# Optimization experiments

Measured on AMD Instinct MI355X. Metric: run time of the kernel, lower is better.

The kernel has to match this reference:

```python
import jax, jax.numpy as jnp
import numpy as np

Q, L = 512, 4096


def setup_inputs() -> dict:
    key = jax.random.key(0)
    ks = jax.random.split(key, 12)
    def rn(k, shape, s=0.05):
        return jax.random.normal(k, shape, jnp.float32) * s
    return {
        "reactions": jax.random.normal(ks[0], (1, Q, 256), jnp.float32),
        "protein":   jax.random.normal(ks[1], (1, L, 1024), jnp.float32),
        # conv1d(1024->256, k=1) == pointwise linear
        "Wc":  rn(ks[2], (256, 1024)), "bc":  jnp.zeros((256,), jnp.float32),
        "W1":  rn(ks[3], (64, 256)),   "b1":  jnp.zeros((64,), jnp.float32),
        "W2":  rn(ks[4], (64, 256)),   "b2":  jnp.zeros((64,), jnp.float32),
        "Wa":  rn(ks[5], (64, 64)),    "ba":  jnp.zeros((64,), jnp.float32),
        "Wpa": rn(ks[6], (64, 64)),    "bpa": jnp.zeros((64,), jnp.float32),
        "Wra": rn(ks[7], (64, 64)),    "bra": jnp.zeros((64,), jnp.float32),
        "Wf1": rn(ks[8], (256, 128)),  "bf1": jnp.zeros((256,), jnp.float32),
        "Wf2": rn(ks[9], (128, 256)),  "bf2": jnp.zeros((128,), jnp.float32),
        "Wf3": rn(ks[10], (1, 128)),   "bf3": jnp.zeros((1,), jnp.float32),
    }


def reference(reactions, protein, Wc, bc, W1, b1, W2, b2, Wa, ba,
              Wpa, bpa, Wra, bra, Wf1, bf1, Wf2, bf2, Wf3, bf3):
    # protein: [1, L, 1024] -> 1x1 conv over channels == linear -> [L, 256]
    p = jax.nn.relu(protein[0] @ Wc.T + bc)
    # reactions: [1, Q, 256] -> [Q, 64]
    r = jax.nn.relu(reactions[0] @ W2.T + b2)
    # protein tokens -> [L, 64]
    k = jax.nn.relu(p @ W1.T + b1)

    ra = r @ Wra.T + bra            # [Q, 64]
    pa = k @ Wpa.T + bpa            # [L, 64]
    # broadcast outer-sum + relu + small linear: [Q, L, 64]
    A = jax.nn.relu(ra[:, None, :] + pa[None, :, :]) @ Wa.T + ba

    r_gate = jax.nn.sigmoid(jnp.mean(A, axis=1))   # [Q, 64]
    p_gate = jax.nn.sigmoid(jnp.mean(A, axis=0))   # [L, 64]

    rxnfp = r + r * r_gate                          # [Q, 64]
    prot = jnp.max(k + k * p_gate, axis=0)          # [64]  maxpool over L

    ctx = jnp.concatenate(
        [rxnfp, jnp.broadcast_to(prot, (rxnfp.shape[0], 64))], axis=1)  # [Q,128]

    # dropout layers are identity in eval mode
    h = jax.nn.leaky_relu(ctx @ Wf1.T + bf1)
    h = jax.nn.leaky_relu(h @ Wf2.T + bf2)
    out = h @ Wf3.T + bf3
    return out.reshape(-1)                          # [Q]
```

## Files before the change

### kernel.cpp

```cpp
#include <hip/hip_runtime.h>
#include <hip/hip_bf16.h>
#include <math.h>

#define TPB 256

typedef __attribute__((ext_vector_type(8))) short s16x8;
typedef __attribute__((ext_vector_type(4))) float f32x4;

#define MFMA16(a, b, c) __builtin_amdgcn_mfma_f32_16x16x32_bf16((a), (b), (c), 0, 0, 0)

constexpr unsigned OFF_P    = 0u;
constexpr unsigned OFF_K    = OFF_P    + 4096u*256u;
constexpr unsigned OFF_PA   = OFF_K    + 4096u*64u;
constexpr unsigned OFF_R    = OFF_PA   + 4096u*64u;
constexpr unsigned OFF_RA   = OFF_R    + 512u*64u;
constexpr unsigned OFF_SR   = OFF_RA   + 512u*64u;
constexpr unsigned OFF_PMAX = OFF_SR   + 512u*64u;

__device__ __forceinline__ short f2bf(float x) {
  union { float f; unsigned u; } v; v.f = x;
  unsigned r = v.u + 0x7FFFu + ((v.u >> 16) & 1u);
  return (short)(r >> 16);
}
__device__ __forceinline__ unsigned pkbf(float a, float b) {
  __hip_bfloat162 h = __float22bfloat162_rn(make_float2(a, b));
  union { __hip_bfloat162 h2; unsigned u; } v; v.h2 = h;
  return v.u;
}
union U8 { s16x8 s; unsigned u[4]; };

__global__ __launch_bounds__(TPB, 2) void k1_gemm(
    const float* __restrict__ prot, const float* __restrict__ Wc,
    const float* __restrict__ bc,   float* __restrict__ ws)
{
  int bid = blockIdx.x;
  int tid = threadIdx.x;
  if (bid >= 512) {
    int tb = bid - 512;
    unsigned base = OFF_SR + (unsigned)tb * 16384u;
#pragma unroll
    for (int it = 0; it < 16; ++it) {
      int idx = it * TPB + tid;
      *(float4*)&ws[base + (unsigned)idx * 4u] = make_float4(0.f, 0.f, 0.f, 0.f);
    }
    if (tb == 1 && tid < 16)
      *(float4*)&ws[OFF_PMAX + tid * 4] = make_float4(0.f, 0.f, 0.f, 0.f);
    return;
  }

  __shared__ __align__(16) short Asm[32 * 72];
  __shared__ __align__(16) short Bsm[64 * 72];

  int m0 = (bid >> 2) * 32;
  int n0 = (bid & 3) * 64;
  int wave = tid >> 6, lane = tid & 63;
  int wm = (wave & 1) * 16, wn = (wave >> 1) * 32;
  int lm = lane & 15, quad = lane >> 4;

  int arow = tid >> 3, aseg = (tid & 7) * 8;
  int brow = tid >> 2, bseg = (tid & 3) * 16;

  const float* Ag = prot + (size_t)(m0 + arow) * 1024 + aseg;
  const float* Bg = Wc   + (size_t)(n0 + brow) * 1024 + bseg;

  float4 a4[2], b4[4];
#pragma unroll
  for (int i = 0; i < 2; ++i) a4[i] = *(const float4*)(Ag + i * 4);
#pragma unroll
  for (int i = 0; i < 4; ++i) b4[i] = *(const float4*)(Bg + i * 4);

  f32x4 acc[2] = {};

  for (int kc = 0; kc < 16; ++kc) {
    __syncthreads();
    {
      U8 s;
      s.u[0] = pkbf(a4[0].x, a4[0].y); s.u[1] = pkbf(a4[0].z, a4[0].w);
      s.u[2] = pkbf(a4[1].x, a4[1].y); s.u[3] = pkbf(a4[1].z, a4[1].w);
      *(s16x8*)&Asm[arow * 72 + aseg] = s.s;
    }
#pragma unroll
    for (int h = 0; h < 2; ++h) {
      U8 s;
      s.u[0] = pkbf(b4[h*2].x,   b4[h*2].y);
      s.u[1] = pkbf(b4[h*2].z,   b4[h*2].w);
      s.u[2] = pkbf(b4[h*2+1].x, b4[h*2+1].y);
      s.u[3] = pkbf(b4[h*2+1].z, b4[h*2+1].w);
      *(s16x8*)&Bsm[brow * 72 + bseg + h * 8] = s.s;
    }
    if (kc < 15) {
#pragma unroll
      for (int i = 0; i < 2; ++i) a4[i] = *(const float4*)(Ag + (kc + 1) * 64 + i * 4);
#pragma unroll
      for (int i = 0; i < 4; ++i) b4[i] = *(const float4*)(Bg + (kc + 1) * 64 + i * 4);
    }
    __syncthreads();
#pragma unroll
    for (int ks = 0; ks < 2; ++ks) {
      s16x8 af = *(const s16x8*)&Asm[(wm + lm) * 72 + ks * 32 + quad * 8];
#pragma unroll
      for (int ni = 0; ni < 2; ++ni) {
        s16x8 bfv = *(const s16x8*)&Bsm[(wn + ni * 16 + lm) * 72 + ks * 32 + quad * 8];
        acc[ni] = MFMA16(af, bfv, acc[ni]);
      }
    }
  }

#pragma unroll
  for (int ni = 0; ni < 2; ++ni) {
    int col = n0 + wn + ni * 16 + lm;
    float bcv = bc[col];
#pragma unroll
    for (int r = 0; r < 4; ++r) {
      int row = m0 + wm + quad * 4 + r;
      ws[OFF_P + (unsigned)row * 256u + col] = fmaxf(acc[ni][r] + bcv, 0.f);
    }
  }
}

__global__ __launch_bounds__(TPB, 2) void k2_heads(
    const float* __restrict__ reactions,
    const float* __restrict__ W1,  const float* __restrict__ b1,
    const float* __restrict__ W2,  const float* __restrict__ b2,
    const float* __restrict__ Wpa, const float* __restrict__ bpa,
    const float* __restrict__ Wra, const float* __restrict__ bra,
    float* __restrict__ ws)
{
  __shared__ __align__(16) short Asm[32 * 264];
  __shared__ __align__(16) short Bsm[64 * 264];
  __shared__ __align__(16) short Ksm[32 * 72];
  __shared__ __align__(16) short Wsm[64 * 72];
  int bid = blockIdx.x, tid = threadIdx.x;
  bool isProt = bid < 128;
  int row0 = (isProt ? bid : (bid - 128)) * 32;
  const float* src  = isProt ? (ws + OFF_P) : reactions;
  const float* Wst1 = isProt ? W1 : W2;
  const float* bv   = isProt ? b1 : b2;
  const float* Wst2 = isProt ? Wpa : Wra;
  const float* b2nd = isProt ? bpa : bra;
  float* out1 = ws + (isProt ? OFF_K : OFF_R);
  float* out2 = ws + (isProt ? OFF_PA : OFF_RA);

  {
    int row = tid >> 3, seg = (tid & 7) * 32;
    const float* sp = src + (size_t)(row0 + row) * 256 + seg;
    float4 f[8];
#pragma unroll
    for (int i = 0; i < 8; ++i) f[i] = *(const float4*)(sp + i * 4);
#pragma unroll
    for (int i = 0; i < 4; ++i) {
      U8 s;
      s.u[0] = pkbf(f[2*i].x,   f[2*i].y);
      s.u[1] = pkbf(f[2*i].z,   f[2*i].w);
      s.u[2] = pkbf(f[2*i+1].x, f[2*i+1].y);
      s.u[3] = pkbf(f[2*i+1].z, f[2*i+1].w);
      *(s16x8*)&Asm[row * 264 + seg + i * 8] = s.s;
    }
  }
  {
    int row = tid >> 2, seg = (tid & 3) * 64;
    const float* sp = Wst1 + (size_t)row * 256 + seg;
#pragma unroll
    for (int i = 0; i < 8; ++i) {
      float4 fa = *(const float4*)(sp + i * 8);
      float4 fb = *(const float4*)(sp + i * 8 + 4);
      U8 s;
      s.u[0] = pkbf(fa.x, fa.y); s.u[1] = pkbf(fa.z, fa.w);
      s.u[2] = pkbf(fb.x, fb.y); s.u[3] = pkbf(fb.z, fb.w);
      *(s16x8*)&Bsm[row * 264 + seg + i * 8] = s.s;
    }
  }
  {
    int row = tid >> 2, seg = (tid & 3) * 16;
    const float* sp = Wst2 + (size_t)row * 64 + seg;
#pragma unroll
    for (int i = 0; i < 2; ++i) {
      float4 fa = *(const float4*)(sp + i * 8);
      float4 fb = *(const float4*)(sp + i * 8 + 4);
      U8 s;
      s.u[0] = pkbf(fa.x, fa.y); s.u[1] = pkbf(fa.z, fa.w);
      s.u[2] = pkbf(fb.x, fb.y); s.u[3] = pkbf(fb.z, fb.w);
      *(s16x8*)&Wsm[row * 72 + seg + i * 8] = s.s;
    }
  }
  __syncthreads();

  int wave = tid >> 6, lane = tid & 63;
  int lm = lane & 15, quad = lane >> 4;
  int wm = (wave >> 1) * 16, wn = (wave & 1) * 32;

  f32x4 acc[2] = {};
#pragma unroll
  for (int kc = 0; kc < 8; ++kc) {
    s16x8 a = *(const s16x8*)&Asm[(wm + lm) * 264 + kc * 32 + quad * 8];
#pragma unroll
    for (int ni = 0; ni < 2; ++ni) {
      s16x8 b = *(const s16x8*)&Bsm[(wn + ni * 16 + lm) * 264 + kc * 32 + quad * 8];
      acc[ni] = MFMA16(a, b, acc[ni]);
    }
  }
#pragma unroll
  for (int ni = 0; ni < 2; ++ni) {
    int col = wn + ni * 16 + lm;
    float bb = bv[col];
#pragma unroll
    for (int r = 0; r < 4; ++r) {
      int row = wm + quad * 4 + r;
      float kv = fmaxf(acc[ni][r] + bb, 0.f);
      out1[(size_t)(row0 + row) * 64 + col] = kv;
      Ksm[row * 72 + col] = f2bf(kv);
    }
  }
  __syncthreads();

  f32x4 acc2[2] = {};
#pragma unroll
  for (int kc = 0; kc < 2; ++kc) {
    s16x8 a = *(const s16x8*)&Ksm[(wm + lm) * 72 + kc * 32 + quad * 8];
#pragma unroll
    for (int ni = 0; ni < 2; ++ni) {
      s16x8 b = *(const s16x8*)&Wsm[(wn + ni * 16 + lm) * 72 + kc * 32 + quad * 8];
      acc2[ni] = MFMA16(a, b, acc2[ni]);
    }
  }
#pragma unroll
  for (int ni = 0; ni < 2; ++ni) {
    int col = wn + ni * 16 + lm;
    float bb = b2nd[col];
#pragma unroll
    for (int r = 0; r < 4; ++r) {
      int row = wm + quad * 4 + r;
      out2[(size_t)(row0 + row) * 64 + col] = acc2[ni][r] + bb;
    }
  }
}

__global__ __launch_bounds__(TPB, 4) void k3_interact(
    const float* __restrict__ Wa, const float* __restrict__ ba,
    float* __restrict__ ws)
{
  __shared__ float sm[8192];
  int bid = blockIdx.x, tid = threadIdx.x;
  int c = tid & 63, g = tid >> 6;
  const float* ra = ws + OFF_RA;
  const float* pa = ws + OFF_PA;

  if (bid < 256) {
    int l0 = bid * 16;
    float v[4], acc[4];
#pragma unroll
    for (int i = 0; i < 4; ++i) {
      v[i] = pa[(unsigned)(l0 + g * 4 + i) * 64u + c];
      acc[i] = 0.f;
    }
    const float* rap = ra + c;
#pragma unroll 8
    for (int q = 0; q < 512; ++q) {
      float x = rap[q * 64];
#pragma unroll
      for (int i = 0; i < 4; ++i) acc[i] += fmaxf(v[i] + x, 0.f);
    }
#pragma unroll
    for (int i = 0; i < 4; ++i) sm[(g * 4 + i) * 64 + c] = acc[i];
    for (int it = 0; it < 16; ++it) {
      int idx = it * TPB + tid;
      int a = idx >> 6, bb = idx & 63;
      sm[1024 + bb * 65 + a] = Wa[idx];
    }
    __syncthreads();
    float vmax = 0.f;
    float bac = ba[c];
#pragma unroll
    for (int i = 0; i < 4; ++i) {
      int ll = g * 4 + i;
      float dot = 0.f;
#pragma unroll 8
      for (int jj = 0; jj < 64; ++jj)
        dot += sm[ll * 64 + jj] * sm[1024 + jj * 65 + c];
      float pg = 1.f / (1.f + __expf(-(dot * (1.f / 512.f) + bac)));
      float val = ws[OFF_K + (unsigned)(l0 + ll) * 64u + c] * (1.f + pg);
      vmax = fmaxf(vmax, val);
    }
    atomicMax((int*)&ws[OFF_PMAX + c], __float_as_int(vmax));
  } else {
    int b = bid - 256;
    int qt = b >> 5, ls = b & 31;
    int q0 = qt * 16, l0 = ls * 128;
    int srow = tid >> 4, sc4 = (tid & 15) * 4;
    const float* src = pa + (size_t)l0 * 64;
#pragma unroll
    for (int it = 0; it < 8; ++it) {
      int row = it * 16 + srow;
      *(float4*)&sm[row * 64 + sc4] = *(const float4*)(src + row * 64 + sc4);
    }
    float u[4], acc[4];
#pragma unroll
    for (int i = 0; i < 4; ++i) {
      u[i] = ra[(unsigned)(q0 + g * 4 + i) * 64u + c];
      acc[i] = 0.f;
    }
    __syncthreads();
#pragma unroll 8
    for (int l = 0; l < 128; ++l) {
      float x = sm[l * 64 + c];
#pragma unroll
      for (int i = 0; i < 4; ++i) acc[i] += fmaxf(u[i] + x, 0.f);
    }
#pragma unroll
    for (int i = 0; i < 4; ++i)
      atomicAdd(&ws[OFF_SR + (unsigned)(q0 + g * 4 + i) * 64u + c], acc[i]);
  }
}

__global__ __launch_bounds__(TPB) void k4_final(
    const float* __restrict__ Wa,  const float* __restrict__ ba,
    const float* __restrict__ Wf1, const float* __restrict__ bf1,
    const float* __restrict__ Wf2, const float* __restrict__ bf2,
    const float* __restrict__ Wf3, const float* __restrict__ bf3,
    float* __restrict__ ws, float* __restrict__ out)
{
  __shared__ __align__(16) short mrb[16 * 72];
  __shared__ __align__(16) short wab[64 * 72];
  __shared__ __align__(16) short ctxb[16 * 136];
  __shared__ __align__(16) short h1b[16 * 264];
  __shared__ __align__(16) short wgt[256 * 136];
  __shared__ float red[64];
  int bid = blockIdx.x, tid = threadIdx.x;
  int q0 = bid * 16;
  int wave = tid >> 6, lane = tid & 63;
  int lm = lane & 15, quad = lane >> 4;

  {
    int q = tid >> 4, c4 = (tid & 15) * 4;
    float4 v = *(const float4*)&ws[OFF_SR + (unsigned)(q0 + q) * 64u + c4];
    uint2 st = make_uint2(pkbf(v.x * (1.f/4096.f), v.y * (1.f/4096.f)),
                          pkbf(v.z * (1.f/4096.f), v.w * (1.f/4096.f)));
    *(uint2*)&mrb[q * 72 + c4] = st;
  }
#pragma unroll
  for (int it = 0; it < 4; ++it) {
    int i4 = it * TPB + tid;
    int row = i4 >> 4, c4 = (i4 & 15) * 4;
    float4 v = *(const float4*)&Wa[row * 64 + c4];
    uint2 st = make_uint2(pkbf(v.x, v.y), pkbf(v.z, v.w));
    *(uint2*)&wab[row * 72 + c4] = st;
  }
  __syncthreads();

  f32x4 gacc = {};
#pragma unroll
  for (int kc = 0; kc < 2; ++kc) {
    s16x8 a = *(const s16x8*)&mrb[lm * 72 + kc * 32 + quad * 8];
    s16x8 b = *(const s16x8*)&wab[(wave * 16 + lm) * 72 + kc * 32 + quad * 8];
    gacc = MFMA16(a, b, gacc);
  }
  {
    int c = wave * 16 + lm;
    float bac = ba[c];
    short pb = f2bf(ws[OFF_PMAX + c]);
#pragma unroll
    for (int r = 0; r < 4; ++r) {
      int q = quad * 4 + r;
      float gg = 1.f / (1.f + __expf(-(gacc[r] + bac)));
      float rv = ws[OFF_R + (unsigned)(q0 + q) * 64u + c];
      ctxb[q * 136 + c]      = f2bf(rv * (1.f + gg));
      ctxb[q * 136 + 64 + c] = pb;
    }
  }
#pragma unroll 4
  for (int it = 0; it < 32; ++it) {
    int i4 = it * TPB + tid;
    int row = i4 >> 5, c4 = (i4 & 31) * 4;
    float4 v = *(const float4*)&Wf1[row * 128 + c4];
    uint2 st = make_uint2(pkbf(v.x, v.y), pkbf(v.z, v.w));
    *(uint2*)&wgt[row * 136 + c4] = st;
  }
  __syncthreads();

  f32x4 h[4] = {};
#pragma unroll
  for (int kc = 0; kc < 4; ++kc) {
    s16x8 a = *(const s16x8*)&ctxb[lm * 136 + kc * 32 + quad * 8];
#pragma unroll
    for (int nt = 0; nt < 4; ++nt) {
      s16x8 b = *(const s16x8*)&wgt[(wave * 64 + nt * 16 + lm) * 136 + kc * 32 + quad * 8];
      h[nt] = MFMA16(a, b, h[nt]);
    }
  }
#pragma unroll
  for (int nt = 0; nt < 4; ++nt) {
    int n = wave * 64 + nt * 16 + lm;
    float bb = bf1[n];
#pragma unroll
    for (int r = 0; r < 4; ++r) {
      int q = quad * 4 + r;
      float v = h[nt][r] + bb;
      v = v > 0.f ? v : 0.01f * v;
      h1b[q * 264 + n] = f2bf(v);
    }
  }
  __syncthreads();

#pragma unroll 4
  for (int it = 0; it < 32; ++it) {
    int i4 = it * TPB + tid;
    int row = i4 >> 6, c4 = (i4 & 63) * 4;
    float4 v = *(const float4*)&Wf2[row * 256 + c4];
    uint2 st = make_uint2(pkbf(v.x, v.y), pkbf(v.z, v.w));
    *(uint2*)&wgt[row * 264 + c4] = st;
  }
  __syncthreads();

  f32x4 o[2] = {};
#pragma unroll
  for (int kc = 0; kc < 8; ++kc) {
    s16x8 a = *(const s16x8*)&h1b[lm * 264 + kc * 32 + quad * 8];
#pragma unroll
    for (int nt = 0; nt < 2; ++nt) {
      s16x8 b = *(const s16x8*)&wgt[(wave * 32 + nt * 16 + lm) * 264 + kc * 32 + quad * 8];
      o[nt] = MFMA16(a, b, o[nt]);
    }
  }
  float pv[4] = {0.f, 0.f, 0.f, 0.f};
#pragma unroll
  for (int nt = 0; nt < 2; ++nt) {
    int m = wave * 32 + nt * 16 + lm;
    float bb = bf2[m], w3 = Wf3[m];
#pragma unroll
    for (int r = 0; r < 4; ++r) {
      float v = o[nt][r] + bb;
      v = v > 0.f ? v : 0.01f * v;
      pv[r] += v * w3;
    }
  }
#pragma unroll
  for (int msk = 1; msk < 16; msk <<= 1)
#pragma unroll
    for (int r = 0; r < 4; ++r) pv[r] += __shfl_xor(pv[r], msk);
  if (lm == 0) {
#pragma unroll
    for (int r = 0; r < 4; ++r) red[(quad * 4 + r) * 4 + wave] = pv[r];
  }
  __syncthreads();
  if (tid < 16)
    out[q0 + tid] = red[tid * 4] + red[tid * 4 + 1] + red[tid * 4 + 2] +
                    red[tid * 4 + 3] + bf3[0];
}

extern "C" void kernel_launch(void* const* d_in, const int* in_sizes, int n_in,
                              void* d_out, int out_size, void* d_ws, size_t ws_size,
                              hipStream_t stream)
{
  const float* reactions = (const float*)d_in[0];
  const float* protein   = (const float*)d_in[1];
  const float* Wc  = (const float*)d_in[2];
  const float* bc  = (const float*)d_in[3];
  const float* W1  = (const float*)d_in[4];
  const float* b1  = (const float*)d_in[5];
  const float* W2  = (const float*)d_in[6];
  const float* b2  = (const float*)d_in[7];
  const float* Wa  = (const float*)d_in[8];
  const float* ba  = (const float*)d_in[9];
  const float* Wpa = (const float*)d_in[10];
  const float* bpa = (const float*)d_in[11];
  const float* Wra = (const float*)d_in[12];
  const float* bra = (const float*)d_in[13];
  const float* Wf1 = (const float*)d_in[14];
  const float* bf1 = (const float*)d_in[15];
  const float* Wf2 = (const float*)d_in[16];
  const float* bf2 = (const float*)d_in[17];
  const float* Wf3 = (const float*)d_in[18];
  const float* bf3 = (const float*)d_in[19];
  float* ws  = (float*)d_ws;
  float* out = (float*)d_out;

  hipLaunchKernelGGL(k1_gemm, dim3(514), dim3(TPB), 0, stream,
                     protein, Wc, bc, ws);
  hipLaunchKernelGGL(k2_heads, dim3(144), dim3(TPB), 0, stream,
                     reactions, W1, b1, W2, b2, Wpa, bpa, Wra, bra, ws);
  hipLaunchKernelGGL(k3_interact, dim3(1280), dim3(TPB), 0, stream,
                     Wa, ba, ws);
  hipLaunchKernelGGL(k4_final, dim3(32), dim3(TPB), 0, stream,
                     Wa, ba, Wf1, bf1, Wf2, bf2, Wf3, bf3, ws, out);
}
```

Before: 172.9 us.

## Split p-gate reduction into balanced tiled atomic blocks plus separate gate kernel

Previously 256 blocks each looped over all 512 queries serially to compute per-L sums, giving long-tail, unbalanced blocks next to the tiled Q-sum blocks. The interaction kernel now uses one uniform tiled block type for both the Q-side and L-side sums, accumulated with atomics into a new zeroed workspace region. The gate/maxpool step moves into a new small kernel. This improves load balance and parallelism, at the cost of an extra kernel launch, more atomics and extra zeroing work in k1.

```diff
diff --git a/kernel.cpp b/kernel.cpp
--- a/kernel.cpp
+++ b/kernel.cpp
@@ -16,6 +16,7 @@
 constexpr unsigned OFF_RA   = OFF_R    + 512u*64u;
 constexpr unsigned OFF_SR   = OFF_RA   + 512u*64u;
 constexpr unsigned OFF_PMAX = OFF_SR   + 512u*64u;
+constexpr unsigned OFF_SP   = OFF_PMAX + 64u;
 
 __device__ __forceinline__ short f2bf(float x) {
   union { float f; unsigned u; } v; v.f = x;
@@ -37,14 +38,23 @@
   int tid = threadIdx.x;
   if (bid >= 512) {
     int tb = bid - 512;
-    unsigned base = OFF_SR + (unsigned)tb * 16384u;
-#pragma unroll
-    for (int it = 0; it < 16; ++it) {
-      int idx = it * TPB + tid;
-      *(float4*)&ws[base + (unsigned)idx * 4u] = make_float4(0.f, 0.f, 0.f, 0.f);
-    }
-    if (tb == 1 && tid < 16)
-      *(float4*)&ws[OFF_PMAX + tid * 4] = make_float4(0.f, 0.f, 0.f, 0.f);
+    if (tb < 2) {
+      unsigned base = OFF_SR + (unsigned)tb * 16384u;
+#pragma unroll
+      for (int it = 0; it < 16; ++it) {
+        int idx = it * TPB + tid;
+        *(float4*)&ws[base + (unsigned)idx * 4u] = make_float4(0.f, 0.f, 0.f, 0.f);
+      }
+      if (tb == 1 && tid < 16)
+        *(float4*)&ws[OFF_PMAX + tid * 4] = make_float4(0.f, 0.f, 0.f, 0.f);
+    } else {
+      unsigned base = OFF_SP + (unsigned)(tb - 2) * 32768u;
+#pragma unroll
+      for (int it = 0; it < 32; ++it) {
+        int idx = it * TPB + tid;
+        *(float4*)&ws[base + (unsigned)idx * 4u] = make_float4(0.f, 0.f, 0.f, 0.f);
+      }
+    }
     return;
   }
 
@@ -235,9 +245,7 @@
   }
 }
 
-__global__ __launch_bounds__(TPB, 4) void k3_interact(
-    const float* __restrict__ Wa, const float* __restrict__ ba,
-    float* __restrict__ ws)
+__global__ __launch_bounds__(TPB, 4) void k3_interact(float* __restrict__ ws)
 {
   __shared__ float sm[8192];
   int bid = blockIdx.x, tid = threadIdx.x;
@@ -245,71 +253,80 @@
   const float* ra = ws + OFF_RA;
   const float* pa = ws + OFF_PA;
 
-  if (bid < 256) {
-    int l0 = bid * 16;
-    float v[4], acc[4];
-#pragma unroll
-    for (int i = 0; i < 4; ++i) {
-      v[i] = pa[(unsigned)(l0 + g * 4 + i) * 64u + c];
-      acc[i] = 0.f;
-    }
-    const float* rap = ra + c;
+  int b = bid >> 1;
+  const float *X, *Y;
+  unsigned x0, y0;
+  float* OUT;
+  if ((bid & 1) == 0) {
+    x0 = (unsigned)(b >> 5) * 16;
+    y0 = (unsigned)(b & 31) * 128;
+    X = ra; Y = pa; OUT = ws + OFF_SR;
+  } else {
+    x0 = (unsigned)(b >> 2) * 16;
+    y0 = (unsigned)(b & 3) * 128;
+    X = pa; Y = ra; OUT = ws + OFF_SP;
+  }
+
+  int srow = tid >> 4, sc4 = (tid & 15) * 4;
+  const float* src = Y + (size_t)y0 * 64;
+#pragma unroll
+  for (int it = 0; it < 8; ++it) {
+    int row = it * 16 + srow;
+    *(float4*)&sm[row * 64 + sc4] = *(const float4*)(src + row * 64 + sc4);
+  }
+  float u[4], acc[4];
+#pragma unroll
+  for (int i = 0; i < 4; ++i) {
+    u[i] = X[(x0 + g * 4 + i) * 64u + c];
+    acc[i] = 0.f;
+  }
+  __syncthreads();
 #pragma unroll 8
-    for (int q = 0; q < 512; ++q) {
-      float x = rap[q * 64];
-#pragma unroll
-      for (int i = 0; i < 4; ++i) acc[i] += fmaxf(v[i] + x, 0.f);
-    }
-#pragma unroll
-    for (int i = 0; i < 4; ++i) sm[(g * 4 + i) * 64 + c] = acc[i];
-    for (int it = 0; it < 16; ++it) {
-      int idx = it * TPB + tid;
-      int a = idx >> 6, bb = idx & 63;
-      sm[1024 + bb * 65 + a] = Wa[idx];
-    }
-    __syncthreads();
-    float vmax = 0.f;
-    float bac = ba[c];
-#pragma unroll
-    for (int i = 0; i < 4; ++i) {
-      int ll = g * 4 + i;
-      float dot = 0.f;
+  for (int l = 0; l < 128; ++l) {
+    float x = sm[l * 64 + c];
+#pragma unroll
+    for (int i = 0; i < 4; ++i) acc[i] += fmaxf(u[i] + x, 0.f);
+  }
+#pragma unroll
+  for (int i = 0; i < 4; ++i)
+    atomicAdd(&OUT[(x0 + g * 4 + i) * 64u + c], acc[i]);
+}
+
+__global__ __launch_bounds__(TPB) void k3b_gate(
+    const float* __restrict__ Wa, const float* __restrict__ ba,
+    float* __restrict__ ws)
+{
+  __shared__ float sp[16 * 64];
+  __shared__ float wat[64 * 65];
+  int bid = blockIdx.x, tid = threadIdx.x;
+  int c = tid & 63, g = tid >> 6;
+  int l0 = bid * 16;
+  {
+    int idx = tid * 4;
+    float4 v = *(const float4*)&ws[OFF_SP + (unsigned)l0 * 64u + idx];
+    v.x *= (1.f / 512.f); v.y *= (1.f / 512.f);
+    v.z *= (1.f / 512.f); v.w *= (1.f / 512.f);
+    *(float4*)&sp[idx] = v;
+  }
+  for (int it = 0; it < 16; ++it) {
+    int idx = it * TPB + tid;
+    wat[(idx & 63) * 65 + (idx >> 6)] = Wa[idx];
+  }
+  __syncthreads();
+  float vmax = 0.f;
+  float bac = ba[c];
+#pragma unroll
+  for (int i = 0; i < 4; ++i) {
+    int ll = g * 4 + i;
+    float dot = 0.f;
 #pragma unroll 8
-      for (int jj = 0; jj < 64; ++jj)
-        dot += sm[ll * 64 + jj] * sm[1024 + jj * 65 + c];
-      float pg = 1.f / (1.f + __expf(-(dot * (1.f / 512.f) + bac)));
-      float val = ws[OFF_K + (unsigned)(l0 + ll) * 64u + c] * (1.f + pg);
-      vmax = fmaxf(vmax, val);
-    }
-    atomicMax((int*)&ws[OFF_PMAX + c], __float_as_int(vmax));
-  } else {
-    int b = bid - 256;
-    int qt = b >> 5, ls = b & 31;
-    int q0 = qt * 16, l0 = ls * 128;
-    int srow = tid >> 4, sc4 = (tid & 15) * 4;
-    const float* src = pa + (size_t)l0 * 64;
-#pragma unroll
-    for (int it = 0; it < 8; ++it) {
-      int row = it * 16 + srow;
-      *(float4*)&sm[row * 64 + sc4] = *(const float4*)(src + row * 64 + sc4);
-    }
-    float u[4], acc[4];
-#pragma unroll
-    for (int i = 0; i < 4; ++i) {
-      u[i] = ra[(unsigned)(q0 + g * 4 + i) * 64u + c];
-      acc[i] = 0.f;
-    }
-    __syncthreads();
-#pragma unroll 8
-    for (int l = 0; l < 128; ++l) {
-      float x = sm[l * 64 + c];
-#pragma unroll
-      for (int i = 0; i < 4; ++i) acc[i] += fmaxf(u[i] + x, 0.f);
-    }
-#pragma unroll
-    for (int i = 0; i < 4; ++i)
-      atomicAdd(&ws[OFF_SR + (unsigned)(q0 + g * 4 + i) * 64u + c], acc[i]);
-  }
+    for (int jj = 0; jj < 64; ++jj)
+      dot += sp[ll * 64 + jj] * wat[jj * 65 + c];
+    float pg = 1.f / (1.f + __expf(-(dot + bac)));
+    float val = ws[OFF_K + (unsigned)(l0 + ll) * 64u + c] * (1.f + pg);
+    vmax = fmaxf(vmax, val);
+  }
+  atomicMax((int*)&ws[OFF_PMAX + c], __float_as_int(vmax));
 }
 
 __global__ __launch_bounds__(TPB) void k4_final(
@@ -474,12 +491,12 @@
   float* ws  = (float*)d_ws;
   float* out = (float*)d_out;
 
-  hipLaunchKernelGGL(k1_gemm, dim3(514), dim3(TPB), 0, stream,
+  hipLaunchKernelGGL(k1_gemm, dim3(522), dim3(TPB), 0, stream,
                      protein, Wc, bc, ws);
   hipLaunchKernelGGL(k2_heads, dim3(144), dim3(TPB), 0, stream,
                      reactions, W1, b1, W2, b2, Wpa, bpa, Wra, bra, ws);
-  hipLaunchKernelGGL(k3_interact, dim3(1280), dim3(TPB), 0, stream,
-                     Wa, ba, ws);
+  hipLaunchKernelGGL(k3_interact, dim3(2048), dim3(TPB), 0, stream, ws);
+  hipLaunchKernelGGL(k3b_gate, dim3(256), dim3(TPB), 0, stream, Wa, ba, ws);
   hipLaunchKernelGGL(k4_final, dim3(32), dim3(TPB), 0, stream,
                      Wa, ba, Wf1, bf1, Wf2, bf2, Wf3, bf3, ws, out);
 }
```

Measured after the change: 174.4 us. About the same (+0.9%).
